# Kernel optimization log

Hardware: AMD Instinct MI355X
Metric: run time of the kernel (lower is better)

## Reference

```python
import jax, jax.numpy as jnp
import numpy as np

N = 50000          # total nodes (types: 20000/17000/13000)
E = 800000         # edges, avg degree 16
NUM_ETYPES = 6
ALPHA = 0.05       # residual-attention blend coefficient
SLOPE = 0.2        # leaky_relu negative slope


def _edge_softmax(e, dst, n):
    # softmax over incoming edges of each destination node; e: [E, H]
    m = jax.ops.segment_max(e, dst, num_segments=n)      # [N, H]
    ex = jnp.exp(e - m[dst])
    s = jax.ops.segment_sum(ex, dst, num_segments=n)     # [N, H]
    return ex / s[dst]


def _gat_layer(h, src, dst, etype, W, We, eemb, al, ar, ae, resW, res_attn, activate):
    n = h.shape[0]
    H, out = al.shape
    feat = (h @ W).reshape(n, H, out)                    # [N, H, out]
    T, edim = eemb.shape
    # edge-type attention term: embedding -> fc_e -> attn_e; only T distinct rows
    et_att = jnp.einsum('thd,hd->th', (eemb @ We).reshape(T, H, edim), ae)  # [T, H]
    el = jnp.einsum('nho,ho->nh', feat, al)              # [N, H]
    er = jnp.einsum('nho,ho->nh', feat, ar)              # [N, H]
    e = jax.nn.leaky_relu(el[src] + er[dst] + et_att[etype], SLOPE)  # [E, H]
    a = _edge_softmax(e, dst, n)                         # [E, H]
    if res_attn is not None:
        a = a * (1.0 - ALPHA) + res_attn * ALPHA
    rst = jax.ops.segment_sum(feat[src] * a[:, :, None], dst, num_segments=n)  # [N, H, out]
    if resW is not None:
        rst = rst + (h @ resW).reshape(n, H, out)
    if activate:
        rst = jax.nn.elu(rst)
    return rst, jax.lax.stop_gradient(a)


def _forward(x0, x1, x2, fcw0, fcb0, fcw1, fcb1, fcw2, fcb2,
             W0, We0, eemb0, al0, ar0, ae0,
             W1, We1, eemb1, al1, ar1, ae1, resW1,
             W2, We2, eemb2, al2, ar2, ae2, resW2,
             src, dst, etype):
    # per-type input projection then concat (feat_drop=0 -> identity)
    h = jnp.concatenate([x0 @ fcw0 + fcb0, x1 @ fcw1 + fcb1, x2 @ fcw2 + fcb2], axis=0)  # [N, 64]
    h1, a = _gat_layer(h, src, dst, etype, W0, We0, eemb0, al0, ar0, ae0, None, None, True)
    h1 = h1.reshape(h1.shape[0], -1)                     # [N, 256]
    h2, a = _gat_layer(h1, src, dst, etype, W1, We1, eemb1, al1, ar1, ae1, resW1, a, True)
    h2 = h2.reshape(h2.shape[0], -1)                     # [N, 256]
    logits, _ = _gat_layer(h2, src, dst, etype, W2, We2, eemb2, al2, ar2, ae2, resW2, None, False)
    return logits                                        # [N, 1, 16]


def setup_inputs():
    key = jax.random.key(0)
    ks = iter(jax.random.split(key, 48))
    def rn(shape, fan_in):
        return jax.random.normal(next(ks), shape, jnp.float32) / np.sqrt(fan_in)
    inp = {}
    inp['x0'] = jax.random.normal(next(ks), (20000, 128), jnp.float32)
    inp['x1'] = jax.random.normal(next(ks), (17000, 256), jnp.float32)
    inp['x2'] = jax.random.normal(next(ks), (13000, 64), jnp.float32)
    inp['fcw0'] = rn((128, 64), 128); inp['fcb0'] = jnp.zeros((64,), jnp.float32)
    inp['fcw1'] = rn((256, 64), 256); inp['fcb1'] = jnp.zeros((64,), jnp.float32)
    inp['fcw2'] = rn((64, 64), 64);   inp['fcb2'] = jnp.zeros((64,), jnp.float32)
    # layer 0: in=64 -> H=8, out=32
    inp['W0'] = rn((64, 256), 64); inp['We0'] = rn((64, 512), 64)
    inp['eemb0'] = rn((NUM_ETYPES, 64), 1.0)
    inp['al0'] = rn((8, 32), 32); inp['ar0'] = rn((8, 32), 32); inp['ae0'] = rn((8, 64), 64)
    # layer 1: in=256 -> H=8, out=32, residual
    inp['W1'] = rn((256, 256), 256); inp['We1'] = rn((64, 512), 64)
    inp['eemb1'] = rn((NUM_ETYPES, 64), 1.0)
    inp['al1'] = rn((8, 32), 32); inp['ar1'] = rn((8, 32), 32); inp['ae1'] = rn((8, 64), 64)
    inp['resW1'] = rn((256, 256), 256)
    # output layer: in=256 -> H=1, out=16, residual
    inp['W2'] = rn((256, 16), 256); inp['We2'] = rn((64, 64), 64)
    inp['eemb2'] = rn((NUM_ETYPES, 64), 1.0)
    inp['al2'] = rn((1, 16), 16); inp['ar2'] = rn((1, 16), 16); inp['ae2'] = rn((1, 64), 64)
    inp['resW2'] = rn((256, 16), 256)
    inp['src'] = jax.random.randint(next(ks), (E,), 0, N)
    inp['dst'] = jax.random.randint(next(ks), (E,), 0, N)
    inp['etype'] = jax.random.randint(next(ks), (E,), 0, NUM_ETYPES)
    return inp


def reference(x0, x1, x2, fcw0, fcb0, fcw1, fcb1, fcw2, fcb2,
              W0, We0, eemb0, al0, ar0, ae0,
              W1, We1, eemb1, al1, ar1, ae1, resW1,
              W2, We2, eemb2, al2, ar2, ae2, resW2,
              src, dst, etype):
    return _forward(x0, x1, x2, fcw0, fcb0, fcw1, fcb1, fcw2, fcb2,
                    W0, We0, eemb0, al0, ar0, ae0,
                    W1, We1, eemb1, al1, ar1, ae1, resW1,
                    W2, We2, eemb2, al2, ar2, ae2, resW2,
                    src, dst, etype)
```

## Files before the change

kernel.cpp:

```cpp
#include <hip/hip_runtime.h>
#include <hip/hip_bf16.h>

#define ALPHA 0.05f
#define SLOPE 0.2f
#define LCAP 128

typedef __attribute__((ext_vector_type(8))) short short8v;
typedef __attribute__((ext_vector_type(8))) unsigned short ushort8v;
typedef __attribute__((ext_vector_type(4))) float floatx4;

__device__ inline ushort f2b(float f) {
    uint u = __float_as_uint(f);
    return (ushort)((u + 0x7fffu + ((u >> 16) & 1u)) >> 16);
}
__device__ inline float b2f(ushort b) { return __uint_as_float(((uint)b) << 16); }

__device__ inline void gload_lds16(const ushort* g, ushort* l) {
    __builtin_amdgcn_global_load_lds(
        (const __attribute__((address_space(1))) uint*)g,
        (__attribute__((address_space(3))) uint*)l, 16, 0, 0);
}


__global__ void hist_kernel(const int* __restrict__ dst, int* __restrict__ counts, int E) {
    int e = blockIdx.x * blockDim.x + threadIdx.x;
    if (e < E) atomicAdd(&counts[dst[e]], 1);
}

__global__ __launch_bounds__(256) void scan_part(const int* __restrict__ counts,
                                                 int* __restrict__ offsets,
                                                 int* __restrict__ partial, int n) {
    __shared__ int sd[256];
    int i = blockIdx.x * 256 + threadIdx.x;
    int v = (i < n) ? counts[i] : 0;
    sd[threadIdx.x] = v;
    __syncthreads();
    for (int off = 1; off < 256; off <<= 1) {
        int t = (threadIdx.x >= off) ? sd[threadIdx.x - off] : 0;
        __syncthreads();
        sd[threadIdx.x] += t;
        __syncthreads();
    }
    if (i < n) offsets[i + 1] = sd[threadIdx.x];
    if (threadIdx.x == 255) partial[blockIdx.x] = sd[255];
}

__global__ __launch_bounds__(256) void scan_top(int* __restrict__ partial, int nb) {
    __shared__ int sd[256];
    int v = (threadIdx.x < nb) ? partial[threadIdx.x] : 0;
    sd[threadIdx.x] = v;
    __syncthreads();
    for (int off = 1; off < 256; off <<= 1) {
        int t = (threadIdx.x >= off) ? sd[threadIdx.x - off] : 0;
        __syncthreads();
        sd[threadIdx.x] += t;
        __syncthreads();
    }
    if (threadIdx.x < nb) partial[threadIdx.x] = sd[threadIdx.x];
}

__global__ __launch_bounds__(256) void scan_add(int* __restrict__ offsets,
                                                int* __restrict__ cursor,
                                                const int* __restrict__ partial, int n) {
    int i = blockIdx.x * 256 + threadIdx.x;
    if (i >= n) return;
    int add = (blockIdx.x > 0) ? partial[blockIdx.x - 1] : 0;
    int v = offsets[i + 1] + add;
    offsets[i + 1] = v;
    if (i + 1 < n) cursor[i + 1] = v;
    if (i == 0) { offsets[0] = 0; cursor[0] = 0; }
}

__global__ void scatter_kernel(const int* __restrict__ src, const int* __restrict__ dst,
                               const int* __restrict__ et, int* __restrict__ cursor,
                               int* __restrict__ se, int E) {
    int e = blockIdx.x * blockDim.x + threadIdx.x;
    if (e >= E) return;
    int d = dst[e];
    int pos = atomicAdd(&cursor[d], 1);
    se[pos] = (src[e] << 3) | et[e];
}


__global__ void wprep(const float* __restrict__ W0f, const float* __restrict__ W1f,
                      const float* __restrict__ WRf,
                      const float* __restrict__ fw0, const float* __restrict__ fw1,
                      const float* __restrict__ fw2,
                      ushort* __restrict__ Wt0, ushort* __restrict__ Wt1,
                      ushort* __restrict__ WtR,
                      ushort* __restrict__ ft0, ushort* __restrict__ ft1,
                      ushort* __restrict__ ft2) {
    int i = blockIdx.x * blockDim.x + threadIdx.x;
    if (i < 16384) {
        int k = i / 256, n = i % 256;
        Wt0[n * 64 + k] = f2b(W0f[i]);
    } else if (i < 16384 + 65536) {
        int j = i - 16384;
        int k = j / 256, n = j % 256;
        Wt1[n * 256 + k] = f2b(W1f[j]);
    } else if (i < 16384 + 2 * 65536) {
        int j = i - 16384 - 65536;
        int k = j / 256, n = j % 256;
        WtR[n * 256 + k] = f2b(WRf[j]);
    } else if (i < 147456 + 8192) {
        int j = i - 147456;
        int k = j / 64, n = j % 64;
        ft0[n * 128 + k] = f2b(fw0[j]);
    } else if (i < 147456 + 8192 + 16384) {
        int j = i - 147456 - 8192;
        int k = j / 64, n = j % 64;
        ft1[n * 256 + k] = f2b(fw1[j]);
    } else if (i < 147456 + 8192 + 16384 + 4096) {
        int j = i - 147456 - 8192 - 16384;
        int k = j / 64, n = j % 64;
        ft2[n * 64 + k] = f2b(fw2[j]);
    }
}


__global__ void xprep(const float* __restrict__ x0, const float* __restrict__ x1,
                      const float* __restrict__ x2, ushort* __restrict__ xb,
                      long t0, long t1, long t2) {
    long i = (long)blockIdx.x * blockDim.x + threadIdx.x;
    float4 v;
    if (i < t0) v = reinterpret_cast<const float4*>(x0)[i];
    else if (i < t0 + t1) v = reinterpret_cast<const float4*>(x1)[i - t0];
    else if (i < t0 + t1 + t2) v = reinterpret_cast<const float4*>(x2)[i - t0 - t1];
    else return;
    ushort4 u = {f2b(v.x), f2b(v.y), f2b(v.z), f2b(v.w)};
    reinterpret_cast<ushort4*>(xb)[i] = u;
}


__global__ __launch_bounds__(512) void etype_all(
    const float* __restrict__ eemb0, const float* __restrict__ We0, const float* __restrict__ ae0, float* __restrict__ out0,
    const float* __restrict__ eemb1, const float* __restrict__ We1, const float* __restrict__ ae1, float* __restrict__ out1,
    const float* __restrict__ eemb2, const float* __restrict__ We2, const float* __restrict__ ae2, float* __restrict__ out2) {
    int layer = blockIdx.x / 6, t = blockIdx.x % 6;
    const float *eemb, *We, *ae;
    float* out;
    int H;
    if (layer == 0)      { eemb = eemb0; We = We0; ae = ae0; out = out0; H = 8; }
    else if (layer == 1) { eemb = eemb1; We = We1; ae = ae1; out = out1; H = 8; }
    else                 { eemb = eemb2; We = We2; ae = ae2; out = out2; H = 1; }
    __shared__ float es[64];
    int j = threadIdx.x;
    if (j < 64) es[j] = eemb[t * 64 + j];
    __syncthreads();
    if (j >= H * 64) return;
    float wsum = 0.f;
#pragma unroll 8
    for (int k = 0; k < 64; ++k) wsum += es[k] * We[k * (H * 64) + j];
    float v = wsum * ae[j];
#pragma unroll
    for (int off = 32; off > 0; off >>= 1) v += __shfl_down(v, off, 64);
    if ((j & 63) == 0) out[t * H + (j >> 6)] = v;
}


template<bool ATTN>
__global__ __launch_bounds__(256) void gemm_bf16(const ushort* __restrict__ A,
                                                 const ushort* __restrict__ Bt,
                                                 ushort* __restrict__ Cb,
                                                 const float* __restrict__ al,
                                                 const float* __restrict__ ar,
                                                 float* __restrict__ el,
                                                 float* __restrict__ er,
                                                 int M, int N, int K) {
    __shared__ ushort As[128 * 32];
    __shared__ ushort Bs[128 * 32];
    int bm = blockIdx.y * 128, bn = blockIdx.x * 128;
    int tid = threadIdx.x;
    int wave = tid >> 6, lane = tid & 63;
    int wm = (wave >> 1) * 64, wn = (wave & 1) * 64;
    int r = tid >> 2, c = (tid & 3) * 8;
    floatx4 acc[4][4] = {};
    for (int k0 = 0; k0 < K; k0 += 32) {
        gload_lds16(&A[(long)(bm + r) * K + k0 + c],       &As[(size_t)tid * 8]);
        gload_lds16(&A[(long)(bm + 64 + r) * K + k0 + c],  &As[(size_t)(256 + tid) * 8]);
        gload_lds16(&Bt[(long)(bn + r) * K + k0 + c],      &Bs[(size_t)tid * 8]);
        gload_lds16(&Bt[(long)(bn + 64 + r) * K + k0 + c], &Bs[(size_t)(256 + tid) * 8]);
        __syncthreads();
        int lr = lane & 15, lk = (lane >> 4) * 8;
        short8v af[4], bfr[4];
#pragma unroll
        for (int i = 0; i < 4; ++i)
            af[i] = *reinterpret_cast<const short8v*>(&As[(wm + i * 16 + lr) * 32 + lk]);
#pragma unroll
        for (int j = 0; j < 4; ++j)
            bfr[j] = *reinterpret_cast<const short8v*>(&Bs[(wn + j * 16 + lr) * 32 + lk]);
#pragma unroll
        for (int i = 0; i < 4; ++i)
#pragma unroll
            for (int j = 0; j < 4; ++j)
                acc[i][j] = __builtin_amdgcn_mfma_f32_16x16x32_bf16(af[i], bfr[j], acc[i][j], 0, 0, 0);
        __syncthreads();
    }
    int col = lane & 15, rbase = (lane >> 4) * 4;
#pragma unroll
    for (int i = 0; i < 4; ++i) {
#pragma unroll
        for (int rr = 0; rr < 4; ++rr) {
            int gm = bm + wm + i * 16 + rbase + rr;
            if (gm >= M) continue;
#pragma unroll
            for (int j = 0; j < 4; ++j) {
                int gn = bn + wn + j * 16 + col;
                Cb[(long)gm * N + gn] = f2b(acc[i][j][rr]);
            }
        }
    }
    if (ATTN) {
        int hA = (bn + wn) >> 5;
        float alv[4], arv[4];
#pragma unroll
        for (int j = 0; j < 4; ++j) {
            int h = hA + (j >> 1);
            int o = (j & 1) * 16 + col;
            alv[j] = al[h * 32 + o];
            arv[j] = ar[h * 32 + o];
        }
#pragma unroll
        for (int i = 0; i < 4; ++i) {
#pragma unroll
            for (int rr = 0; rr < 4; ++rr) {
                float slA = acc[i][0][rr] * alv[0] + acc[i][1][rr] * alv[1];
                float slB = acc[i][2][rr] * alv[2] + acc[i][3][rr] * alv[3];
                float srA = acc[i][0][rr] * arv[0] + acc[i][1][rr] * arv[1];
                float srB = acc[i][2][rr] * arv[2] + acc[i][3][rr] * arv[3];
#pragma unroll
                for (int off = 1; off < 16; off <<= 1) {
                    slA += __shfl_xor(slA, off, 64);
                    slB += __shfl_xor(slB, off, 64);
                    srA += __shfl_xor(srA, off, 64);
                    srB += __shfl_xor(srB, off, 64);
                }
                int gm = bm + wm + i * 16 + rbase + rr;
                if (col == 0 && gm < M) {
                    el[gm * 8 + hA]     = slA;
                    el[gm * 8 + hA + 1] = slB;
                    er[gm * 8 + hA]     = srA;
                    er[gm * 8 + hA + 1] = srB;
                }
            }
        }
    }
}


__global__ __launch_bounds__(256) void gemm_dual(const ushort* __restrict__ A,
                                                 const ushort* __restrict__ B1,
                                                 const ushort* __restrict__ B2,
                                                 ushort* __restrict__ C1,
                                                 ushort* __restrict__ C2,
                                                 const float* __restrict__ al,
                                                 const float* __restrict__ ar,
                                                 float* __restrict__ el,
                                                 float* __restrict__ er,
                                                 int M, int N, int K) {
    __shared__ ushort As[128 * 32];
    __shared__ ushort Bs1[128 * 32];
    __shared__ ushort Bs2[128 * 32];
    int bm = blockIdx.y * 128, bn = blockIdx.x * 128;
    int tid = threadIdx.x;
    int wave = tid >> 6, lane = tid & 63;
    int wm = (wave >> 1) * 64, wn = (wave & 1) * 64;
    int r = tid >> 2, c = (tid & 3) * 8;
    floatx4 acc1[4][4] = {};
    floatx4 acc2[4][4] = {};
    for (int k0 = 0; k0 < K; k0 += 32) {
        gload_lds16(&A[(long)(bm + r) * K + k0 + c],        &As[(size_t)tid * 8]);
        gload_lds16(&A[(long)(bm + 64 + r) * K + k0 + c],   &As[(size_t)(256 + tid) * 8]);
        gload_lds16(&B1[(long)(bn + r) * K + k0 + c],       &Bs1[(size_t)tid * 8]);
        gload_lds16(&B1[(long)(bn + 64 + r) * K + k0 + c],  &Bs1[(size_t)(256 + tid) * 8]);
        gload_lds16(&B2[(long)(bn + r) * K + k0 + c],       &Bs2[(size_t)tid * 8]);
        gload_lds16(&B2[(long)(bn + 64 + r) * K + k0 + c],  &Bs2[(size_t)(256 + tid) * 8]);
        __syncthreads();
        int lr = lane & 15, lk = (lane >> 4) * 8;
        short8v af[4], bfr[4];
#pragma unroll
        for (int i = 0; i < 4; ++i)
            af[i] = *reinterpret_cast<const short8v*>(&As[(wm + i * 16 + lr) * 32 + lk]);
#pragma unroll
        for (int j = 0; j < 4; ++j)
            bfr[j] = *reinterpret_cast<const short8v*>(&Bs1[(wn + j * 16 + lr) * 32 + lk]);
#pragma unroll
        for (int i = 0; i < 4; ++i)
#pragma unroll
            for (int j = 0; j < 4; ++j)
                acc1[i][j] = __builtin_amdgcn_mfma_f32_16x16x32_bf16(af[i], bfr[j], acc1[i][j], 0, 0, 0);
#pragma unroll
        for (int j = 0; j < 4; ++j)
            bfr[j] = *reinterpret_cast<const short8v*>(&Bs2[(wn + j * 16 + lr) * 32 + lk]);
#pragma unroll
        for (int i = 0; i < 4; ++i)
#pragma unroll
            for (int j = 0; j < 4; ++j)
                acc2[i][j] = __builtin_amdgcn_mfma_f32_16x16x32_bf16(af[i], bfr[j], acc2[i][j], 0, 0, 0);
        __syncthreads();
    }
    int col = lane & 15, rbase = (lane >> 4) * 4;
#pragma unroll
    for (int i = 0; i < 4; ++i) {
#pragma unroll
        for (int rr = 0; rr < 4; ++rr) {
            int gm = bm + wm + i * 16 + rbase + rr;
            if (gm >= M) continue;
#pragma unroll
            for (int j = 0; j < 4; ++j) {
                int gn = bn + wn + j * 16 + col;
                C1[(long)gm * N + gn] = f2b(acc1[i][j][rr]);
                C2[(long)gm * N + gn] = f2b(acc2[i][j][rr]);
            }
        }
    }
    int hA = (bn + wn) >> 5;
    float alv[4], arv[4];
#pragma unroll
    for (int j = 0; j < 4; ++j) {
        int h = hA + (j >> 1);
        int o = (j & 1) * 16 + col;
        alv[j] = al[h * 32 + o];
        arv[j] = ar[h * 32 + o];
    }
#pragma unroll
    for (int i = 0; i < 4; ++i) {
#pragma unroll
        for (int rr = 0; rr < 4; ++rr) {
            float slA = acc1[i][0][rr] * alv[0] + acc1[i][1][rr] * alv[1];
            float slB = acc1[i][2][rr] * alv[2] + acc1[i][3][rr] * alv[3];
            float srA = acc1[i][0][rr] * arv[0] + acc1[i][1][rr] * arv[1];
            float srB = acc1[i][2][rr] * arv[2] + acc1[i][3][rr] * arv[3];
#pragma unroll
            for (int off = 1; off < 16; off <<= 1) {
                slA += __shfl_xor(slA, off, 64);
                slB += __shfl_xor(slB, off, 64);
                srA += __shfl_xor(srA, off, 64);
                srB += __shfl_xor(srB, off, 64);
            }
            int gm = bm + wm + i * 16 + rbase + rr;
            if (col == 0 && gm < M) {
                el[gm * 8 + hA]     = slA;
                el[gm * 8 + hA + 1] = slB;
                er[gm * 8 + hA]     = srA;
                er[gm * 8 + hA + 1] = srB;
            }
        }
    }
}


__global__ __launch_bounds__(256) void gemm_fc(const ushort* __restrict__ xb,
                                               const ushort* __restrict__ ft0,
                                               const ushort* __restrict__ ft1,
                                               const ushort* __restrict__ ft2,
                                               const float* __restrict__ b0,
                                               const float* __restrict__ b1,
                                               const float* __restrict__ b2,
                                               ushort* __restrict__ C,
                                               int n0, int n1, int n2) {
    int z = blockIdx.z;
    const ushort *A, *Bt;
    const float* bias;
    int M, K;
    long coff;
    if (z == 0)      { A = xb; Bt = ft0; bias = b0; M = n0; K = 128; coff = 0; }
    else if (z == 1) { A = xb + (long)n0 * 128; Bt = ft1; bias = b1; M = n1; K = 256; coff = (long)n0 * 64; }
    else             { A = xb + (long)n0 * 128 + (long)n1 * 256; Bt = ft2; bias = b2; M = n2; K = 64; coff = (long)(n0 + n1) * 64; }
    int bm = blockIdx.y * 128;
    if (bm >= M) return;
    __shared__ ushort As[128 * 32];
    __shared__ ushort Bs[64 * 32];
    int tid = threadIdx.x;
    int wave = tid >> 6, lane = tid & 63;
    int wm = (wave >> 1) * 64, wn = (wave & 1) * 32;
    int r = tid >> 2, c = (tid & 3) * 8;
    floatx4 acc[4][2] = {};
    for (int k0 = 0; k0 < K; k0 += 32) {
        gload_lds16(&A[(long)(bm + r) * K + k0 + c],      &As[(size_t)tid * 8]);
        gload_lds16(&A[(long)(bm + 64 + r) * K + k0 + c], &As[(size_t)(256 + tid) * 8]);
        gload_lds16(&Bt[(long)r * K + k0 + c],            &Bs[(size_t)tid * 8]);
        __syncthreads();
        int lr = lane & 15, lk = (lane >> 4) * 8;
        short8v af[4], bfr[2];
#pragma unroll
        for (int i = 0; i < 4; ++i)
            af[i] = *reinterpret_cast<const short8v*>(&As[(wm + i * 16 + lr) * 32 + lk]);
#pragma unroll
        for (int j = 0; j < 2; ++j)
            bfr[j] = *reinterpret_cast<const short8v*>(&Bs[(wn + j * 16 + lr) * 32 + lk]);
#pragma unroll
        for (int i = 0; i < 4; ++i)
#pragma unroll
            for (int j = 0; j < 2; ++j)
                acc[i][j] = __builtin_amdgcn_mfma_f32_16x16x32_bf16(af[i], bfr[j], acc[i][j], 0, 0, 0);
        __syncthreads();
    }
    int col = lane & 15, rbase = (lane >> 4) * 4;
#pragma unroll
    for (int i = 0; i < 4; ++i) {
#pragma unroll
        for (int rr = 0; rr < 4; ++rr) {
            int gm = bm + wm + i * 16 + rbase + rr;
            if (gm >= M) continue;
#pragma unroll
            for (int j = 0; j < 2; ++j) {
                int gn = wn + j * 16 + col;
                C[coff + (long)gm * 64 + gn] = f2b(acc[i][j][rr] + bias[gn]);
            }
        }
    }
}


__global__ __launch_bounds__(256) void matmul_n16_dual(const ushort* __restrict__ A,
                                                       const float* __restrict__ W2,
                                                       const float* __restrict__ WR,
                                                       ushort* __restrict__ feat2b,
                                                       float* __restrict__ resout,
                                                       const float* __restrict__ al,
                                                       const float* __restrict__ ar,
                                                       float* __restrict__ el,
                                                       float* __restrict__ er, int M) {
    __shared__ float Ws2[256 * 16];
    __shared__ float WsR[256 * 16];
    for (int i = threadIdx.x; i < 256 * 16; i += 256) {
        Ws2[i] = W2[i];
        WsR[i] = WR[i];
    }
    __syncthreads();
    int nn = threadIdx.x % 16;
    float alv = al[nn], arv = ar[nn];
#pragma unroll
    for (int rb = 0; rb < 2; ++rb) {
        int m = blockIdx.x * 32 + rb * 16 + threadIdx.x / 16;
        if (m >= M) continue;
        float s1 = 0.f, s2 = 0.f;
        for (int k8 = 0; k8 < 32; ++k8) {
            uint4 v = *reinterpret_cast<const uint4*>(&A[(long)m * 256 + k8 * 8]);
            const uint* vp = reinterpret_cast<const uint*>(&v);
#pragma unroll
            for (int q = 0; q < 4; ++q) {
                uint w2 = vp[q];
                float f0 = __uint_as_float((w2 & 0xffffu) << 16);
                float f1 = __uint_as_float(w2 & 0xffff0000u);
                int k = k8 * 8 + q * 2;
                s1 += f0 * Ws2[(k + 0) * 16 + nn] + f1 * Ws2[(k + 1) * 16 + nn];
                s2 += f0 * WsR[(k + 0) * 16 + nn] + f1 * WsR[(k + 1) * 16 + nn];
            }
        }
        feat2b[(long)m * 16 + nn] = f2b(s1);
        resout[(long)m * 16 + nn] = s2;
        float sl = s1 * alv, sr = s1 * arv;
#pragma unroll
        for (int off = 1; off < 16; off <<= 1) {
            sl += __shfl_xor(sl, off, 64);
            sr += __shfl_xor(sr, off, 64);
        }
        if (nn == 0) { el[m] = sl; er[m] = sr; }
    }
}


template<bool BLEND, bool SAVE, bool RES>
__global__ __launch_bounds__(64) void fused_edge_h8(
    const int* __restrict__ offsets, const int* __restrict__ se,
    const float* __restrict__ el, const float* __restrict__ er,
    const float* __restrict__ etatt,
    const ushort* __restrict__ featb,
    const ushort* __restrict__ a0_in, ushort* __restrict__ a0_out,
    const ushort* __restrict__ resin, ushort* __restrict__ outb, int N) {
    int d = blockIdx.x;
    int lane = threadIdx.x;
    int lo = offsets[d], hi = offsets[d + 1];
    int deg = hi - lo;
    __shared__ float a_lds[LCAP][8];
    __shared__ int   s_lds[LCAP];
    __shared__ float er_s[8];
    __shared__ float m_s[8], inv_s[8];
    if (lane < 8) er_s[lane] = er[d * 8 + lane];
    __syncthreads();
    bool fast = (deg <= LCAP);
    int half = lane >> 5, t = lane & 31;
    int h8 = t >> 2;
    uint4 pf[4];
    int npf = 0;
    if (fast) {
        for (int i = lane; i < deg * 8; i += 64) {
            int p = i >> 3, h = i & 7;
            int v0 = se[lo + p];
            int s = v0 >> 3, tt = v0 & 7;
            if (h == 0) s_lds[p] = s;
            float v = el[s * 8 + h] + er_s[h] + etatt[tt * 8 + h];
            a_lds[p][h] = v > 0.f ? v : SLOPE * v;
        }
        __syncthreads();
#pragma unroll
        for (int u = 0; u < 4; ++u) {
            int p = half + 2 * u;
            if (p < deg) {
                pf[u] = *reinterpret_cast<const uint4*>(&featb[(long)s_lds[p] * 256 + t * 8]);
                npf = u + 1;
            }
        }
        {
            int g = lane >> 3, h = lane & 7;
            float m = -INFINITY;
            for (int p = g; p < deg; p += 8) m = fmaxf(m, a_lds[p][h]);
#pragma unroll
            for (int off = 8; off < 64; off <<= 1) m = fmaxf(m, __shfl_xor(m, off, 64));
            float ssum = 0.f;
            for (int p = g; p < deg; p += 8) ssum += __expf(a_lds[p][h] - m);
#pragma unroll
            for (int off = 8; off < 64; off <<= 1) ssum += __shfl_xor(ssum, off, 64);
            if (g == 0) {
                m_s[h] = m;
                inv_s[h] = ssum > 0.f ? 1.f / ssum : 0.f;
            }
        }
        __syncthreads();
        for (int i = lane; i < deg * 8; i += 64) {
            int p = i >> 3, h = i & 7;
            float a = __expf(a_lds[p][h] - m_s[h]) * inv_s[h];
            if (BLEND) a = a * (1.f - ALPHA) + b2f(a0_in[lo * 8 + i]) * ALPHA;
            a_lds[p][h] = a;
            if (SAVE) a0_out[lo * 8 + i] = f2b(a);
        }
        __syncthreads();
    } else {
        int g = lane >> 3, h = lane & 7;
        float m = -INFINITY;
        for (int p = g; p < deg; p += 8) {
            int v0 = se[lo + p];
            int s = v0 >> 3, tt = v0 & 7;
            float v = el[s * 8 + h] + er_s[h] + etatt[tt * 8 + h];
            v = v > 0.f ? v : SLOPE * v;
            m = fmaxf(m, v);
        }
#pragma unroll
        for (int off = 8; off < 64; off <<= 1) m = fmaxf(m, __shfl_xor(m, off, 64));
        float ssum = 0.f;
        for (int p = g; p < deg; p += 8) {
            int v0 = se[lo + p];
            int s = v0 >> 3, tt = v0 & 7;
            float v = el[s * 8 + h] + er_s[h] + etatt[tt * 8 + h];
            v = v > 0.f ? v : SLOPE * v;
            ssum += __expf(v - m);
        }
#pragma unroll
        for (int off = 8; off < 64; off <<= 1) ssum += __shfl_xor(ssum, off, 64);
        if (g == 0) {
            m_s[h] = m;
            inv_s[h] = ssum > 0.f ? 1.f / ssum : 0.f;
        }
        __syncthreads();
        if (SAVE) {
            for (int i = lane; i < deg * 8; i += 64) {
                int p = i >> 3, hh = i & 7;
                int v0 = se[lo + p];
                int s = v0 >> 3, tt = v0 & 7;
                float v = el[s * 8 + hh] + er_s[hh] + etatt[tt * 8 + hh];
                v = v > 0.f ? v : SLOPE * v;
                float a = __expf(v - m_s[hh]) * inv_s[hh];
                if (BLEND) a = a * (1.f - ALPHA) + b2f(a0_in[lo * 8 + i]) * ALPHA;
                a0_out[lo * 8 + i] = f2b(a);
            }
        }
    }
    float acc[8];
#pragma unroll
    for (int k = 0; k < 8; ++k) acc[k] = 0.f;
    if (RES && half == 0) {
        uint4 rv = *reinterpret_cast<const uint4*>(&resin[(long)d * 256 + t * 8]);
        const uint* rp = reinterpret_cast<const uint*>(&rv);
#pragma unroll
        for (int q = 0; q < 4; ++q) {
            acc[2 * q]     = __uint_as_float(rp[q] << 16);
            acc[2 * q + 1] = __uint_as_float(rp[q] & 0xffff0000u);
        }
    }
    if (fast) {
#pragma unroll
        for (int u = 0; u < 4; ++u) {
            if (u < npf) {
                float a = a_lds[half + 2 * u][h8];
                const uint* fp = reinterpret_cast<const uint*>(&pf[u]);
#pragma unroll
                for (int q = 0; q < 4; ++q) {
                    acc[2 * q]     += __uint_as_float(fp[q] << 16) * a;
                    acc[2 * q + 1] += __uint_as_float(fp[q] & 0xffff0000u) * a;
                }
            }
        }
        int p = half + 8;
        for (; p + 6 < deg; p += 8) {
            int s0 = s_lds[p],     s1 = s_lds[p + 2];
            int s2 = s_lds[p + 4], s3 = s_lds[p + 6];
            float a0 = a_lds[p][h8],     a1 = a_lds[p + 2][h8];
            float a2 = a_lds[p + 4][h8], a3 = a_lds[p + 6][h8];
            uint4 f0 = *reinterpret_cast<const uint4*>(&featb[(long)s0 * 256 + t * 8]);
            uint4 f1 = *reinterpret_cast<const uint4*>(&featb[(long)s1 * 256 + t * 8]);
            uint4 f2 = *reinterpret_cast<const uint4*>(&featb[(long)s2 * 256 + t * 8]);
            uint4 f3 = *reinterpret_cast<const uint4*>(&featb[(long)s3 * 256 + t * 8]);
            const uint* q0 = reinterpret_cast<const uint*>(&f0);
            const uint* q1 = reinterpret_cast<const uint*>(&f1);
            const uint* q2 = reinterpret_cast<const uint*>(&f2);
            const uint* q3 = reinterpret_cast<const uint*>(&f3);
#pragma unroll
            for (int q = 0; q < 4; ++q) {
                acc[2 * q] += __uint_as_float(q0[q] << 16) * a0
                            + __uint_as_float(q1[q] << 16) * a1
                            + __uint_as_float(q2[q] << 16) * a2
                            + __uint_as_float(q3[q] << 16) * a3;
                acc[2 * q + 1] += __uint_as_float(q0[q] & 0xffff0000u) * a0
                                + __uint_as_float(q1[q] & 0xffff0000u) * a1
                                + __uint_as_float(q2[q] & 0xffff0000u) * a2
                                + __uint_as_float(q3[q] & 0xffff0000u) * a3;
            }
        }
        for (; p < deg; p += 2) {
            int s = s_lds[p];
            float a = a_lds[p][h8];
            uint4 fv = *reinterpret_cast<const uint4*>(&featb[(long)s * 256 + t * 8]);
            const uint* fp = reinterpret_cast<const uint*>(&fv);
#pragma unroll
            for (int q = 0; q < 4; ++q) {
                uint u = fp[q];
                acc[2 * q]     += __uint_as_float(u << 16) * a;
                acc[2 * q + 1] += __uint_as_float(u & 0xffff0000u) * a;
            }
        }
    } else {
        for (int p = half; p < deg; p += 2) {
            int v0 = se[lo + p];
            int s = v0 >> 3, tt = v0 & 7;
            float v = el[s * 8 + h8] + er_s[h8] + etatt[tt * 8 + h8];
            v = v > 0.f ? v : SLOPE * v;
            float a = __expf(v - m_s[h8]) * inv_s[h8];
            if (BLEND) a = a * (1.f - ALPHA) + b2f(a0_in[(long)(lo + p) * 8 + h8]) * ALPHA;
            uint4 fv = *reinterpret_cast<const uint4*>(&featb[(long)s * 256 + t * 8]);
            const uint* fp = reinterpret_cast<const uint*>(&fv);
#pragma unroll
            for (int q = 0; q < 4; ++q) {
                uint u = fp[q];
                acc[2 * q]     += __uint_as_float(u << 16) * a;
                acc[2 * q + 1] += __uint_as_float(u & 0xffff0000u) * a;
            }
        }
    }
#pragma unroll
    for (int k = 0; k < 8; ++k) acc[k] += __shfl_down(acc[k], 32);
    if (half == 0) {
        ushort8v o;
#pragma unroll
        for (int k = 0; k < 8; ++k) {
            float v = acc[k];
            v = v > 0.f ? v : __expf(v) - 1.f;
            o[k] = f2b(v);
        }
        *reinterpret_cast<ushort8v*>(&outb[(long)d * 256 + t * 8]) = o;
    }
}


__global__ __launch_bounds__(64) void fused_edge_h1(
    const int* __restrict__ offsets, const int* __restrict__ se,
    const float* __restrict__ el, const float* __restrict__ er,
    const float* __restrict__ etatt,
    const ushort* __restrict__ featb2, const float* __restrict__ resout,
    float* __restrict__ out, int N) {
    int d = blockIdx.x;
    int lane = threadIdx.x;
    int lo = offsets[d], hi = offsets[d + 1];
    int deg = hi - lo;
    __shared__ float a_lds[512];
    float er_d = er[d];
    bool fast = (deg <= 512);
    float m = -INFINITY, inv = 0.f;
    if (fast) {
        for (int i = lane; i < deg; i += 64) {
            int v0 = se[lo + i];
            int s = v0 >> 3, t = v0 & 7;
            float v = el[s] + er_d + etatt[t];
            a_lds[i] = v > 0.f ? v : SLOPE * v;
        }
        __syncthreads();
        for (int i = lane; i < deg; i += 64) m = fmaxf(m, a_lds[i]);
#pragma unroll
        for (int off = 1; off < 64; off <<= 1) m = fmaxf(m, __shfl_xor(m, off, 64));
        float ssum = 0.f;
        for (int i = lane; i < deg; i += 64) ssum += __expf(a_lds[i] - m);
#pragma unroll
        for (int off = 1; off < 64; off <<= 1) ssum += __shfl_xor(ssum, off, 64);
        inv = ssum > 0.f ? 1.f / ssum : 0.f;
        for (int i = lane; i < deg; i += 64) a_lds[i] = __expf(a_lds[i] - m) * inv;
        __syncthreads();
    } else {
        for (int i = lane; i < deg; i += 64) {
            int v0 = se[lo + i];
            int s = v0 >> 3, t = v0 & 7;
            float v = el[s] + er_d + etatt[t];
            v = v > 0.f ? v : SLOPE * v;
            m = fmaxf(m, v);
        }
#pragma unroll
        for (int off = 1; off < 64; off <<= 1) m = fmaxf(m, __shfl_xor(m, off, 64));
        float ssum = 0.f;
        for (int i = lane; i < deg; i += 64) {
            int v0 = se[lo + i];
            int s = v0 >> 3, t = v0 & 7;
            float v = el[s] + er_d + etatt[t];
            v = v > 0.f ? v : SLOPE * v;
            ssum += __expf(v - m);
        }
#pragma unroll
        for (int off = 1; off < 64; off <<= 1) ssum += __shfl_xor(ssum, off, 64);
        inv = ssum > 0.f ? 1.f / ssum : 0.f;
    }
    int g = lane >> 1, t = lane & 1;
    float acc[8];
#pragma unroll
    for (int k = 0; k < 8; ++k) acc[k] = 0.f;
    for (int p = g; p < deg; p += 32) {
        int v0 = se[lo + p];
        int s = v0 >> 3;
        float a;
        if (fast) a = a_lds[p];
        else {
            int tt = v0 & 7;
            float v = el[s] + er_d + etatt[tt];
            v = v > 0.f ? v : SLOPE * v;
            a = __expf(v - m) * inv;
        }
        uint4 fv = *reinterpret_cast<const uint4*>(&featb2[(long)s * 16 + t * 8]);
        const uint* fp = reinterpret_cast<const uint*>(&fv);
#pragma unroll
        for (int q = 0; q < 4; ++q) {
            acc[2 * q]     += __uint_as_float(fp[q] << 16) * a;
            acc[2 * q + 1] += __uint_as_float(fp[q] & 0xffff0000u) * a;
        }
    }
#pragma unroll
    for (int off = 2; off < 64; off <<= 1)
#pragma unroll
        for (int k = 0; k < 8; ++k) acc[k] += __shfl_down(acc[k], off);
    if (lane < 2) {
        const float* rp = &resout[(long)d * 16 + t * 8];
        float4 r0 = *reinterpret_cast<const float4*>(rp);
        float4 r1 = *reinterpret_cast<const float4*>(rp + 4);
        float* op = &out[(long)d * 16 + t * 8];
        *reinterpret_cast<float4*>(op)     = make_float4(acc[0] + r0.x, acc[1] + r0.y, acc[2] + r0.z, acc[3] + r0.w);
        *reinterpret_cast<float4*>(op + 4) = make_float4(acc[4] + r1.x, acc[5] + r1.y, acc[6] + r1.z, acc[7] + r1.w);
    }
}


extern "C" void kernel_launch(void* const* d_in, const int* in_sizes, int n_in,
                              void* d_out, int out_size, void* d_ws, size_t ws_size,
                              hipStream_t stream) {
    const float* x0   = (const float*)d_in[0];
    const float* x1   = (const float*)d_in[1];
    const float* x2   = (const float*)d_in[2];
    const float* fcw0 = (const float*)d_in[3];
    const float* fcb0 = (const float*)d_in[4];
    const float* fcw1 = (const float*)d_in[5];
    const float* fcb1 = (const float*)d_in[6];
    const float* fcw2 = (const float*)d_in[7];
    const float* fcb2 = (const float*)d_in[8];
    const float* W0   = (const float*)d_in[9];
    const float* We0  = (const float*)d_in[10];
    const float* eemb0= (const float*)d_in[11];
    const float* al0  = (const float*)d_in[12];
    const float* ar0  = (const float*)d_in[13];
    const float* ae0  = (const float*)d_in[14];
    const float* W1   = (const float*)d_in[15];
    const float* We1  = (const float*)d_in[16];
    const float* eemb1= (const float*)d_in[17];
    const float* al1  = (const float*)d_in[18];
    const float* ar1  = (const float*)d_in[19];
    const float* ae1  = (const float*)d_in[20];
    const float* resW1= (const float*)d_in[21];
    const float* W2   = (const float*)d_in[22];
    const float* We2  = (const float*)d_in[23];
    const float* eemb2= (const float*)d_in[24];
    const float* al2  = (const float*)d_in[25];
    const float* ar2  = (const float*)d_in[26];
    const float* ae2  = (const float*)d_in[27];
    const float* resW2= (const float*)d_in[28];
    const int* src    = (const int*)d_in[29];
    const int* dst    = (const int*)d_in[30];
    const int* etype  = (const int*)d_in[31];

    const int n0 = in_sizes[0] / 128;
    const int n1 = in_sizes[1] / 256;
    const int n2 = in_sizes[2] / 64;
    const int N  = n0 + n1 + n2;
    const int E  = in_sizes[29];
    const long s0 = in_sizes[0], s1 = in_sizes[1], s2 = in_sizes[2];

    char* w = (char*)d_ws;
    auto alloc = [&](size_t bytes) {
        char* p = w;
        w += (bytes + 255) & ~(size_t)255;
        return p;
    };
    int*    counts  = (int*)alloc((size_t)N * 4);
    int*    offsets = (int*)alloc((size_t)(N + 1) * 4);
    int*    cursor  = (int*)alloc((size_t)N * 4);
    int*    partial = (int*)alloc(1024 * 4);
    int*    se      = (int*)alloc((size_t)E * 4);
    ushort* h2res   = (ushort*)alloc((size_t)N * 256 * 2);
    ushort* a0b     = (ushort*)alloc((size_t)E * 8 * 2);
    ushort* xb      = (ushort*)alloc((size_t)(s0 + s1 + s2) * 2 + 128 * 256 * 2);
    ushort* h0bf    = (ushort*)alloc((size_t)N * 64 * 2 + 128 * 256 * 2);
    ushort* featb   = (ushort*)alloc((size_t)N * 256 * 2);
    ushort* h1bf    = (ushort*)alloc((size_t)N * 256 * 2 + 128 * 256 * 2);
    ushort* h2bf    = (ushort*)alloc((size_t)N * 256 * 2);
    float*  el      = (float*)alloc((size_t)N * 8 * 4);
    float*  er      = (float*)alloc((size_t)N * 8 * 4);
    float*  etatt0  = (float*)alloc(64 * 4);
    float*  etatt1  = (float*)alloc(64 * 4);
    float*  etatt2  = (float*)alloc(64 * 4);
    ushort* Wt0     = (ushort*)alloc((size_t)256 * 64 * 2);
    ushort* Wt1     = (ushort*)alloc((size_t)256 * 256 * 2);
    ushort* WtR     = (ushort*)alloc((size_t)256 * 256 * 2);
    ushort* ft0     = (ushort*)alloc((size_t)64 * 128 * 2);
    ushort* ft1     = (ushort*)alloc((size_t)64 * 256 * 2);
    ushort* ft2     = (ushort*)alloc((size_t)64 * 64 * 2);
    ushort* feat2b  = (ushort*)alloc((size_t)N * 16 * 2);
    float*  resout  = (float*)alloc((size_t)N * 16 * 4);
    float*  out     = (float*)d_out;

    const int TB = 256;
    int eb = (E + TB - 1) / TB;
    int nb1 = (N + 255) / 256;

    hipMemsetAsync(counts, 0, (size_t)N * 4, stream);
    hist_kernel<<<eb, TB, 0, stream>>>(dst, counts, E);
    scan_part<<<nb1, 256, 0, stream>>>(counts, offsets, partial, N);
    scan_top<<<1, 256, 0, stream>>>(partial, nb1);
    scan_add<<<nb1, 256, 0, stream>>>(offsets, cursor, partial, N);
    scatter_kernel<<<eb, TB, 0, stream>>>(src, dst, etype, cursor, se, E);

    wprep<<<(176128 + TB - 1) / TB, TB, 0, stream>>>(W0, W1, resW1, fcw0, fcw1, fcw2,
                                                     Wt0, Wt1, WtR, ft0, ft1, ft2);
    etype_all<<<18, 512, 0, stream>>>(eemb0, We0, ae0, etatt0,
                                      eemb1, We1, ae1, etatt1,
                                      eemb2, We2, ae2, etatt2);
    long tot4 = (s0 + s1 + s2) / 4;
    xprep<<<(int)((tot4 + TB - 1) / TB), TB, 0, stream>>>(x0, x1, x2, xb, s0 / 4, s1 / 4, s2 / 4);

    {
        int maxM = n0 > n1 ? n0 : n1;
        if (n2 > maxM) maxM = n2;
        dim3 g(1, (maxM + 127) / 128, 3);
        gemm_fc<<<g, TB, 0, stream>>>(xb, ft0, ft1, ft2, fcb0, fcb1, fcb2, h0bf, n0, n1, n2);
    }

    dim3 gg(256 / 128, (N + 127) / 128);

    gemm_bf16<true><<<gg, TB, 0, stream>>>(h0bf, Wt0, featb, al0, ar0, el, er, N, 256, 64);
    fused_edge_h8<false, true, false><<<N, 64, 0, stream>>>(
        offsets, se, el, er, etatt0, featb, nullptr, a0b, nullptr, h1bf, N);

    gemm_dual<<<gg, TB, 0, stream>>>(h1bf, Wt1, WtR, featb, h2res, al1, ar1, el, er, N, 256, 256);
    fused_edge_h8<true, false, true><<<N, 64, 0, stream>>>(
        offsets, se, el, er, etatt1, featb, a0b, nullptr, h2res, h2bf, N);

    matmul_n16_dual<<<(N + 31) / 32, TB, 0, stream>>>(
        h2bf, W2, resW2, feat2b, resout, al2, ar2, el, er, N);
    fused_edge_h1<<<N, 64, 0, stream>>>(offsets, se, el, er, etatt2, feat2b, resout, out, N);
}
```

Before: 419.1 us.

## Fuse input bf16 conversion into fc GEMM and use MFMA for output-layer projection

Removes the separate xprep pass: gemm_fc now reads the fp32 inputs directly, converts them to bf16 in registers and stores them to LDS, which saves one write and one read of the converted input array. Separately, the scalar fp32 output-layer projection (W2 and resW2, N=16 each) is replaced by an MFMA bf16 GEMM. The two weight matrices are pre-transposed into one combined bf16 buffer by wprep, and the el/er reductions are fused into the epilogue. The trade-offs are lower precision for the residual projection and synchronous loads in place of async LDS loads for the A operand.

```diff
diff --git a/kernel.cpp b/kernel.cpp
--- a/kernel.cpp
+++ b/kernel.cpp
@@ -86,10 +86,11 @@
                       const float* __restrict__ WRf,
                       const float* __restrict__ fw0, const float* __restrict__ fw1,
                       const float* __restrict__ fw2,
+                      const float* __restrict__ W2f, const float* __restrict__ WR2f,
                       ushort* __restrict__ Wt0, ushort* __restrict__ Wt1,
                       ushort* __restrict__ WtR,
                       ushort* __restrict__ ft0, ushort* __restrict__ ft1,
-                      ushort* __restrict__ ft2) {
+                      ushort* __restrict__ ft2, ushort* __restrict__ Wt2R) {
     int i = blockIdx.x * blockDim.x + threadIdx.x;
     if (i < 16384) {
         int k = i / 256, n = i % 256;
@@ -114,21 +115,15 @@
         int j = i - 147456 - 8192 - 16384;
         int k = j / 64, n = j % 64;
         ft2[n * 64 + k] = f2b(fw2[j]);
-    }
-}
-
-
-__global__ void xprep(const float* __restrict__ x0, const float* __restrict__ x1,
-                      const float* __restrict__ x2, ushort* __restrict__ xb,
-                      long t0, long t1, long t2) {
-    long i = (long)blockIdx.x * blockDim.x + threadIdx.x;
-    float4 v;
-    if (i < t0) v = reinterpret_cast<const float4*>(x0)[i];
-    else if (i < t0 + t1) v = reinterpret_cast<const float4*>(x1)[i - t0];
-    else if (i < t0 + t1 + t2) v = reinterpret_cast<const float4*>(x2)[i - t0 - t1];
-    else return;
-    ushort4 u = {f2b(v.x), f2b(v.y), f2b(v.z), f2b(v.w)};
-    reinterpret_cast<ushort4*>(xb)[i] = u;
+    } else if (i < 176128 + 4096) {
+        int j = i - 176128;
+        int k = j / 16, n = j % 16;
+        Wt2R[n * 256 + k] = f2b(W2f[j]);
+    } else if (i < 176128 + 8192) {
+        int j = i - 176128 - 4096;
+        int k = j / 16, n = j % 16;
+        Wt2R[(16 + n) * 256 + k] = f2b(WR2f[j]);
+    }
 }
 
 
@@ -350,7 +345,9 @@
 }
 
 
-__global__ __launch_bounds__(256) void gemm_fc(const ushort* __restrict__ xb,
+__global__ __launch_bounds__(256) void gemm_fc(const float* __restrict__ x0,
+                                               const float* __restrict__ x1,
+                                               const float* __restrict__ x2,
                                                const ushort* __restrict__ ft0,
                                                const ushort* __restrict__ ft1,
                                                const ushort* __restrict__ ft2,
@@ -360,13 +357,14 @@
                                                ushort* __restrict__ C,
                                                int n0, int n1, int n2) {
     int z = blockIdx.z;
-    const ushort *A, *Bt;
+    const float* A;
+    const ushort* Bt;
     const float* bias;
     int M, K;
     long coff;
-    if (z == 0)      { A = xb; Bt = ft0; bias = b0; M = n0; K = 128; coff = 0; }
-    else if (z == 1) { A = xb + (long)n0 * 128; Bt = ft1; bias = b1; M = n1; K = 256; coff = (long)n0 * 64; }
-    else             { A = xb + (long)n0 * 128 + (long)n1 * 256; Bt = ft2; bias = b2; M = n2; K = 64; coff = (long)(n0 + n1) * 64; }
+    if (z == 0)      { A = x0; Bt = ft0; bias = b0; M = n0; K = 128; coff = 0; }
+    else if (z == 1) { A = x1; Bt = ft1; bias = b1; M = n1; K = 256; coff = (long)n0 * 64; }
+    else             { A = x2; Bt = ft2; bias = b2; M = n2; K = 64;  coff = (long)(n0 + n1) * 64; }
     int bm = blockIdx.y * 128;
     if (bm >= M) return;
     __shared__ ushort As[128 * 32];
@@ -377,9 +375,26 @@
     int r = tid >> 2, c = (tid & 3) * 8;
     floatx4 acc[4][2] = {};
     for (int k0 = 0; k0 < K; k0 += 32) {
-        gload_lds16(&A[(long)(bm + r) * K + k0 + c],      &As[(size_t)tid * 8]);
-        gload_lds16(&A[(long)(bm + 64 + r) * K + k0 + c], &As[(size_t)(256 + tid) * 8]);
-        gload_lds16(&Bt[(long)r * K + k0 + c],            &Bs[(size_t)tid * 8]);
+        {
+            int gm0 = bm + r, gm1 = bm + 64 + r;
+            ushort8v u0 = {0, 0, 0, 0, 0, 0, 0, 0};
+            ushort8v u1 = {0, 0, 0, 0, 0, 0, 0, 0};
+            if (gm0 < M) {
+                float4 lo = *reinterpret_cast<const float4*>(&A[(long)gm0 * K + k0 + c]);
+                float4 hi = *reinterpret_cast<const float4*>(&A[(long)gm0 * K + k0 + c + 4]);
+                u0[0] = f2b(lo.x); u0[1] = f2b(lo.y); u0[2] = f2b(lo.z); u0[3] = f2b(lo.w);
+                u0[4] = f2b(hi.x); u0[5] = f2b(hi.y); u0[6] = f2b(hi.z); u0[7] = f2b(hi.w);
+            }
+            if (gm1 < M) {
+                float4 lo = *reinterpret_cast<const float4*>(&A[(long)gm1 * K + k0 + c]);
+                float4 hi = *reinterpret_cast<const float4*>(&A[(long)gm1 * K + k0 + c + 4]);
+                u1[0] = f2b(lo.x); u1[1] = f2b(lo.y); u1[2] = f2b(lo.z); u1[3] = f2b(lo.w);
+                u1[4] = f2b(hi.x); u1[5] = f2b(hi.y); u1[6] = f2b(hi.z); u1[7] = f2b(hi.w);
+            }
+            *reinterpret_cast<ushort8v*>(&As[(size_t)tid * 8]) = u0;
+            *reinterpret_cast<ushort8v*>(&As[(size_t)(256 + tid) * 8]) = u1;
+        }
+        gload_lds16(&Bt[(long)r * K + k0 + c], &Bs[(size_t)tid * 8]);
         __syncthreads();
         int lr = lane & 15, lk = (lane >> 4) * 8;
         short8v af[4], bfr[2];
@@ -413,51 +428,65 @@
 }
 
 
-__global__ __launch_bounds__(256) void matmul_n16_dual(const ushort* __restrict__ A,
-                                                       const float* __restrict__ W2,
-                                                       const float* __restrict__ WR,
-                                                       ushort* __restrict__ feat2b,
-                                                       float* __restrict__ resout,
-                                                       const float* __restrict__ al,
-                                                       const float* __restrict__ ar,
-                                                       float* __restrict__ el,
-                                                       float* __restrict__ er, int M) {
-    __shared__ float Ws2[256 * 16];
-    __shared__ float WsR[256 * 16];
-    for (int i = threadIdx.x; i < 256 * 16; i += 256) {
-        Ws2[i] = W2[i];
-        WsR[i] = WR[i];
-    }
+__global__ __launch_bounds__(256) void gemm_small(const ushort* __restrict__ A,
+                                                  const ushort* __restrict__ Wt2R,
+                                                  ushort* __restrict__ feat2b,
+                                                  float* __restrict__ resout,
+                                                  const float* __restrict__ al,
+                                                  const float* __restrict__ ar,
+                                                  float* __restrict__ el,
+                                                  float* __restrict__ er, int M) {
+    __shared__ ushort As[128 * 32];
+    __shared__ ushort Bs[32 * 256];
+    int tid = threadIdx.x;
+    int wave = tid >> 6, lane = tid & 63;
+    int bm = blockIdx.x * 128;
+    for (int i = tid; i < 32 * 256 / 8; i += 256)
+        *reinterpret_cast<ushort8v*>(&Bs[(size_t)i * 8]) =
+            *reinterpret_cast<const ushort8v*>(&Wt2R[(size_t)i * 8]);
     __syncthreads();
-    int nn = threadIdx.x % 16;
-    float alv = al[nn], arv = ar[nn];
-#pragma unroll
-    for (int rb = 0; rb < 2; ++rb) {
-        int m = blockIdx.x * 32 + rb * 16 + threadIdx.x / 16;
-        if (m >= M) continue;
-        float s1 = 0.f, s2 = 0.f;
-        for (int k8 = 0; k8 < 32; ++k8) {
-            uint4 v = *reinterpret_cast<const uint4*>(&A[(long)m * 256 + k8 * 8]);
-            const uint* vp = reinterpret_cast<const uint*>(&v);
-#pragma unroll
-            for (int q = 0; q < 4; ++q) {
-                uint w2 = vp[q];
-                float f0 = __uint_as_float((w2 & 0xffffu) << 16);
-                float f1 = __uint_as_float(w2 & 0xffff0000u);
-                int k = k8 * 8 + q * 2;
-                s1 += f0 * Ws2[(k + 0) * 16 + nn] + f1 * Ws2[(k + 1) * 16 + nn];
-                s2 += f0 * WsR[(k + 0) * 16 + nn] + f1 * WsR[(k + 1) * 16 + nn];
-            }
-        }
-        feat2b[(long)m * 16 + nn] = f2b(s1);
-        resout[(long)m * 16 + nn] = s2;
-        float sl = s1 * alv, sr = s1 * arv;
-#pragma unroll
-        for (int off = 1; off < 16; off <<= 1) {
-            sl += __shfl_xor(sl, off, 64);
-            sr += __shfl_xor(sr, off, 64);
-        }
-        if (nn == 0) { el[m] = sl; er[m] = sr; }
+    int r = tid >> 2, c = (tid & 3) * 8;
+    floatx4 acc[2][2] = {};
+    for (int k0 = 0; k0 < 256; k0 += 32) {
+        gload_lds16(&A[(long)(bm + r) * 256 + k0 + c],      &As[(size_t)tid * 8]);
+        gload_lds16(&A[(long)(bm + 64 + r) * 256 + k0 + c], &As[(size_t)(256 + tid) * 8]);
+        __syncthreads();
+        int lr = lane & 15, lk = (lane >> 4) * 8;
+        short8v af[2], bfr[2];
+#pragma unroll
+        for (int i = 0; i < 2; ++i)
+            af[i] = *reinterpret_cast<const short8v*>(&As[(wave * 32 + i * 16 + lr) * 32 + lk]);
+#pragma unroll
+        for (int j = 0; j < 2; ++j)
+            bfr[j] = *reinterpret_cast<const short8v*>(&Bs[(j * 16 + lr) * 256 + k0 + lk]);
+#pragma unroll
+        for (int i = 0; i < 2; ++i)
+#pragma unroll
+            for (int j = 0; j < 2; ++j)
+                acc[i][j] = __builtin_amdgcn_mfma_f32_16x16x32_bf16(af[i], bfr[j], acc[i][j], 0, 0, 0);
+        __syncthreads();
+    }
+    int col = lane & 15, rbase = (lane >> 4) * 4;
+    float alv = al[col], arv = ar[col];
+#pragma unroll
+    for (int i = 0; i < 2; ++i) {
+#pragma unroll
+        for (int rr = 0; rr < 4; ++rr) {
+            int gm = bm + wave * 32 + i * 16 + rbase + rr;
+            float s1 = acc[i][0][rr];
+            float s2 = acc[i][1][rr];
+            float sl = s1 * alv, sr = s1 * arv;
+#pragma unroll
+            for (int off = 1; off < 16; off <<= 1) {
+                sl += __shfl_xor(sl, off, 64);
+                sr += __shfl_xor(sr, off, 64);
+            }
+            if (gm < M) {
+                feat2b[(long)gm * 16 + col] = f2b(s1);
+                resout[(long)gm * 16 + col] = s2;
+                if (col == 0) { el[gm] = sl; er[gm] = sr; }
+            }
+        }
     }
 }
 
@@ -796,7 +825,6 @@
     const int n2 = in_sizes[2] / 64;
     const int N  = n0 + n1 + n2;
     const int E  = in_sizes[29];
-    const long s0 = in_sizes[0], s1 = in_sizes[1], s2 = in_sizes[2];
 
     char* w = (char*)d_ws;
     auto alloc = [&](size_t bytes) {
@@ -811,11 +839,10 @@
     int*    se      = (int*)alloc((size_t)E * 4);
     ushort* h2res   = (ushort*)alloc((size_t)N * 256 * 2);
     ushort* a0b     = (ushort*)alloc((size_t)E * 8 * 2);
-    ushort* xb      = (ushort*)alloc((size_t)(s0 + s1 + s2) * 2 + 128 * 256 * 2);
     ushort* h0bf    = (ushort*)alloc((size_t)N * 64 * 2 + 128 * 256 * 2);
     ushort* featb   = (ushort*)alloc((size_t)N * 256 * 2);
     ushort* h1bf    = (ushort*)alloc((size_t)N * 256 * 2 + 128 * 256 * 2);
-    ushort* h2bf    = (ushort*)alloc((size_t)N * 256 * 2);
+    ushort* h2bf    = (ushort*)alloc((size_t)N * 256 * 2 + 128 * 256 * 2);
     float*  el      = (float*)alloc((size_t)N * 8 * 4);
     float*  er      = (float*)alloc((size_t)N * 8 * 4);
     float*  etatt0  = (float*)alloc(64 * 4);
@@ -827,6 +854,7 @@
     ushort* ft0     = (ushort*)alloc((size_t)64 * 128 * 2);
     ushort* ft1     = (ushort*)alloc((size_t)64 * 256 * 2);
     ushort* ft2     = (ushort*)alloc((size_t)64 * 64 * 2);
+    ushort* Wt2R    = (ushort*)alloc((size_t)32 * 256 * 2);
     ushort* feat2b  = (ushort*)alloc((size_t)N * 16 * 2);
     float*  resout  = (float*)alloc((size_t)N * 16 * 4);
     float*  out     = (float*)d_out;
@@ -842,19 +870,19 @@
     scan_add<<<nb1, 256, 0, stream>>>(offsets, cursor, partial, N);
     scatter_kernel<<<eb, TB, 0, stream>>>(src, dst, etype, cursor, se, E);
 
-    wprep<<<(176128 + TB - 1) / TB, TB, 0, stream>>>(W0, W1, resW1, fcw0, fcw1, fcw2,
-                                                     Wt0, Wt1, WtR, ft0, ft1, ft2);
+    wprep<<<(184320 + TB - 1) / TB, TB, 0, stream>>>(W0, W1, resW1, fcw0, fcw1, fcw2,
+                                                     W2, resW2,
+                                                     Wt0, Wt1, WtR, ft0, ft1, ft2, Wt2R);
     etype_all<<<18, 512, 0, stream>>>(eemb0, We0, ae0, etatt0,
                                       eemb1, We1, ae1, etatt1,
                                       eemb2, We2, ae2, etatt2);
-    long tot4 = (s0 + s1 + s2) / 4;
-    xprep<<<(int)((tot4 + TB - 1) / TB), TB, 0, stream>>>(x0, x1, x2, xb, s0 / 4, s1 / 4, s2 / 4);
 
     {
         int maxM = n0 > n1 ? n0 : n1;
         if (n2 > maxM) maxM = n2;
         dim3 g(1, (maxM + 127) / 128, 3);
-        gemm_fc<<<g, TB, 0, stream>>>(xb, ft0, ft1, ft2, fcb0, fcb1, fcb2, h0bf, n0, n1, n2);
+        gemm_fc<<<g, TB, 0, stream>>>(x0, x1, x2, ft0, ft1, ft2, fcb0, fcb1, fcb2,
+                                      h0bf, n0, n1, n2);
     }
 
     dim3 gg(256 / 128, (N + 127) / 128);
@@ -867,7 +895,7 @@
     fused_edge_h8<true, false, true><<<N, 64, 0, stream>>>(
         offsets, se, el, er, etatt1, featb, a0b, nullptr, h2res, h2bf, N);
 
-    matmul_n16_dual<<<(N + 31) / 32, TB, 0, stream>>>(
-        h2bf, W2, resW2, feat2b, resout, al2, ar2, el, er, N);
+    gemm_small<<<(N + 127) / 128, TB, 0, stream>>>(
+        h2bf, Wt2R, feat2b, resout, al2, ar2, el, er, N);
     fused_edge_h1<<<N, 64, 0, stream>>>(offsets, se, el, er, etatt2, feat2b, resout, out, N);
 }
```

Measured after the change: 394.9 us (median of 2 runs). 1.06x faster.
